# Optimization experiments

Hardware: AMD Instinct MI355X
Metric: run time of the kernel (lower is better)

Reference implementation:

```python
import jax, jax.numpy as jnp
import numpy as np

B, S, D, H, R, N, RK = 2, 2048, 1024, 16, 64, 32, 128
DH = D // H
EPS = 1e-5


def setup_inputs() -> dict:
    key = jax.random.key(0)
    ks = jax.random.split(key, 24)
    f = lambda i, shape, sc=1.0: jax.random.normal(ks[i], shape, dtype=jnp.float32) * sc
    sm = lambda i, shape: jax.nn.softmax(f(i, shape), axis=-1)
    return {
        'x': f(0, (B, S, D)),
        'f_qk': f(1, (N, D, R), 0.02), 'f_v': f(2, (N, D, R), 0.02),
        'r_qk': f(3, (N, R, D), 0.02), 'r_v': f(4, (N, R, D), 0.02),
        'f_know': f(5, (N, D, RK), 0.02), 'r_know': f(6, (N, RK, D), 0.02),
        'W_O': f(7, (D, D), 0.02),
        'gamma1': jnp.ones(D, jnp.float32), 'beta1': jnp.zeros(D, jnp.float32),
        'gamma2': jnp.ones(D, jnp.float32), 'beta2': jnp.zeros(D, jnp.float32),
        'w_fq': sm(8, (B, S, N)), 'w_fk': sm(9, (B, S, N)), 'w_fv': sm(10, (B, S, N)),
        'w_rq': sm(11, (B, S, N)), 'w_rk': sm(12, (B, S, N)), 'w_rv': sm(13, (B, S, N)),
        'w_know_f': sm(14, (B, S, N)), 'w_know_r': sm(15, (B, S, N)),
    }


def _ln(x, g, b):
    mu = jnp.mean(x, axis=-1, keepdims=True)
    var = jnp.mean(jnp.square(x - mu), axis=-1, keepdims=True)
    return g * (x - mu) * jax.lax.rsqrt(var + EPS) + b


def _feature(x, neurons, w):
    # x [B,S,D], neurons [N,D,R], w [B,S,N] -> [B,S,R]
    all_h = jnp.einsum('bsd,ndr->bsnr', x, neurons)
    return jnp.einsum('bsnr,bsn->bsr', all_h, w)


def _restore(h, neurons, w):
    # h [B,S,R], neurons [N,R,D], w [B,S,N] -> [B,S,D]
    # fuse: avoid materializing [B,S,N,D]; outer-product [B,S,N,R] is small
    t = w[..., None] * h[:, :, None, :]
    return jnp.einsum('bsnr,nrd->bsd', t, neurons)


def _causal_attn(Q, K, V):
    # Q,K,V: [B,H,S,DH]
    scale = 1.0 / jnp.sqrt(jnp.asarray(DH, Q.dtype))
    scores = jnp.einsum('bhqd,bhkd->bhqk', Q, K) * scale
    mask = jnp.tril(jnp.ones((S, S), bool))
    scores = jnp.where(mask, scores, jnp.asarray(-jnp.inf, scores.dtype))
    probs = jax.nn.softmax(scores, axis=-1)
    return jnp.einsum('bhqk,bhkd->bhqd', probs, V)


def reference(x, f_qk, f_v, r_qk, r_v, f_know, r_know, W_O,
              gamma1, beta1, gamma2, beta2,
              w_fq, w_fk, w_fv, w_rq, w_rk, w_rv, w_know_f, w_know_r):
    # --- attention circuit ---
    nx = _ln(x, gamma1, beta1)
    h_q = _feature(nx, f_qk, w_fq)
    h_k = _feature(nx, f_qk, w_fk)
    h_v = _feature(nx, f_v, w_fv)
    Q = _restore(h_q, r_qk, w_rq)
    K = _restore(h_k, r_qk, w_rk)
    V = _restore(h_v, r_v, w_rv)
    to_heads = lambda t: t.reshape(B, S, H, DH).transpose(0, 2, 1, 3)
    attn = _causal_attn(to_heads(Q), to_heads(K), to_heads(V))
    attn = attn.transpose(0, 2, 1, 3).reshape(B, S, D)
    attn_out = attn @ W_O.T  # nn.Linear(d_model, d_model, bias=False)
    x = x + attn_out
    # --- knowledge circuit ---
    nx2 = _ln(x, gamma2, beta2)
    h = _feature(nx2, f_know, w_know_f)
    know_out = _restore(h, r_know, w_know_r)
    x = x + know_out
    return x
```

## Files before the change

### kernel.cpp

```cpp
#include <hip/hip_runtime.h>
#include <stdint.h>


typedef __bf16 bf16x8 __attribute__((ext_vector_type(8)));
typedef float f32x4 __attribute__((ext_vector_type(4)));

__device__ __forceinline__ unsigned short f2b(float f) {
  union { float f; unsigned u; } v; v.f = f;
  unsigned u = v.u;
  unsigned r = (u + 0x7FFFu + ((u >> 16) & 1u)) >> 16;
  return (unsigned short)r;
}
__device__ __forceinline__ float b2f(unsigned short h) {
  union { unsigned u; float f; } v; v.u = ((unsigned)h) << 16;
  return v.f;
}
__device__ __forceinline__ unsigned pk2(float lo, float hi) {
  return (unsigned)f2b(lo) | ((unsigned)f2b(hi) << 16);
}
__device__ __forceinline__ unsigned pkt(float lo, float hi) {
  union { float f; unsigned u; } a, b; a.f = lo; b.f = hi;
  return __builtin_amdgcn_perm(b.u, a.u, 0x07060302u);
}
__device__ __forceinline__ f32x4 vmax4(f32x4 a, f32x4 b) {
  f32x4 r;
  r[0] = fmaxf(a[0], b[0]); r[1] = fmaxf(a[1], b[1]);
  r[2] = fmaxf(a[2], b[2]); r[3] = fmaxf(a[3], b[3]);
  return r;
}

#define PHASE(M0) { \
  const bf16x8 a00 = *(const bf16x8*)&lsA[cur][(wr * 128 + (M0) * 16 + l16) * 64 + sl0]; \
  const bf16x8 a01 = *(const bf16x8*)&lsA[cur][(wr * 128 + (M0) * 16 + l16) * 64 + sl1]; \
  const bf16x8 a10 = *(const bf16x8*)&lsA[cur][(wr * 128 + (M0 + 1) * 16 + l16) * 64 + sl0]; \
  const bf16x8 a11 = *(const bf16x8*)&lsA[cur][(wr * 128 + (M0 + 1) * 16 + l16) * 64 + sl1]; \
  __builtin_amdgcn_s_setprio(1); \
  _Pragma("unroll") \
  for (int n = 0; n < 4; ++n) { \
    acc[M0][n] = __builtin_amdgcn_mfma_f32_16x16x32_bf16(a00, bfr[n][0], acc[M0][n], 0, 0, 0); \
    acc[M0][n] = __builtin_amdgcn_mfma_f32_16x16x32_bf16(a01, bfr[n][1], acc[M0][n], 0, 0, 0); \
    acc[M0 + 1][n] = __builtin_amdgcn_mfma_f32_16x16x32_bf16(a10, bfr[n][0], acc[M0 + 1][n], 0, 0, 0); \
    acc[M0 + 1][n] = __builtin_amdgcn_mfma_f32_16x16x32_bf16(a11, bfr[n][1], acc[M0 + 1][n], 0, 0, 0); \
  } \
  __builtin_amdgcn_s_setprio(0); }

__global__ __launch_bounds__(512, 2) void gemm_bt256(
    const unsigned short* __restrict__ A, const unsigned short* __restrict__ Bt,
    unsigned short* __restrict__ out, int K) {
  __shared__ unsigned short lsA[2][256 * 64];
  __shared__ unsigned short lsB[2][256 * 64];
  const int N = 4096;
  const int bid = blockIdx.x;
  const int xcd = bid & 7, j = bid >> 3;
  const int row0 = (xcd * 2 + (j >> 4)) * 256;
  const int col0 = (j & 15) * 256;
  const int tid = threadIdx.x;
  const int w = tid >> 6, lane = tid & 63;
  const int quad = lane >> 4, l16 = lane & 15;
  const int wr = w >> 2, wc = w & 3;

  const int scg = ((lane & 7) ^ (lane >> 3)) * 8;
  const unsigned short* apg = A + (size_t)(row0 + w * 8 + (lane >> 3)) * K + scg;
  const unsigned short* bpg = Bt + (size_t)(col0 + w * 8 + (lane >> 3)) * K + scg;

  const int sl0 = (quad ^ (l16 & 7)) * 8;
  const int sl1 = ((4 + quad) ^ (l16 & 7)) * 8;

  const f32x4 fz = {0.f, 0.f, 0.f, 0.f};
  f32x4 acc[8][4];
#pragma unroll
  for (int m = 0; m < 8; ++m)
#pragma unroll
    for (int n = 0; n < 4; ++n) acc[m][n] = fz;

  auto stA = [&](int b, int i, int k0) {
    __builtin_amdgcn_global_load_lds(
        (const __attribute__((address_space(1))) unsigned int*)(apg + (size_t)(i * 64) * K + k0),
        (__attribute__((address_space(3))) unsigned int*)&lsA[b][(i * 64 + w * 8) * 64],
        16, 0, 0);
  };
  auto stB = [&](int b, int i, int k0) {
    __builtin_amdgcn_global_load_lds(
        (const __attribute__((address_space(1))) unsigned int*)(bpg + (size_t)(i * 64) * K + k0),
        (__attribute__((address_space(3))) unsigned int*)&lsB[b][(i * 64 + w * 8) * 64],
        16, 0, 0);
  };

  const int T = K >> 6;
  stA(0, 0, 0); stA(0, 2, 0);
  stB(0, 0, 0); stB(0, 1, 0); stB(0, 2, 0); stB(0, 3, 0);
  stA(0, 1, 0); stA(0, 3, 0);

  for (int t = 0; t < T; ++t) {
    const int cur = t & 1, nxt = cur ^ 1;
    const int k1 = (t + 1) << 6;
    const bool pf = (t + 1 < T);
    asm volatile("s_waitcnt vmcnt(2)" ::: "memory");
    __builtin_amdgcn_s_barrier();
    if (pf) { stA(nxt, 0, k1); stA(nxt, 2, k1); }
    bf16x8 bfr[4][2];
#pragma unroll
    for (int n = 0; n < 4; ++n) {
      bfr[n][0] = *(const bf16x8*)&lsB[cur][(wc * 64 + n * 16 + l16) * 64 + sl0];
      bfr[n][1] = *(const bf16x8*)&lsB[cur][(wc * 64 + n * 16 + l16) * 64 + sl1];
    }
    PHASE(0)
    if (pf) { stB(nxt, 0, k1); stB(nxt, 1, k1); }
    PHASE(2)
    if (pf) { asm volatile("s_waitcnt vmcnt(4)" ::: "memory"); }
    else    { asm volatile("s_waitcnt vmcnt(0)" ::: "memory"); }
    __builtin_amdgcn_s_barrier();
    if (pf) { stB(nxt, 2, k1); stB(nxt, 3, k1); }
    PHASE(4)
    if (pf) { stA(nxt, 1, k1); stA(nxt, 3, k1); }
    PHASE(6)
  }

  const int rb = row0 + wr * 128;
  const int cb = col0 + wc * 64;
#pragma unroll
  for (int m = 0; m < 8; ++m) {
#pragma unroll
    for (int n = 0; n < 4; ++n) {
      const int r = rb + m * 16 + quad * 4;
      const int c = cb + n * 16 + l16;
#pragma unroll
      for (int i = 0; i < 4; ++i)
        out[(size_t)(r + i) * N + c] = f2b(acc[m][n][i]);
    }
  }
}

__global__ __launch_bounds__(256, 3) void gemm_qkv(
    const unsigned short* __restrict__ t_qk, const unsigned short* __restrict__ t_v,
    const unsigned short* __restrict__ r_qkT, const unsigned short* __restrict__ r_vT,
    unsigned short* __restrict__ QK, unsigned short* __restrict__ VT) {
  __shared__ unsigned short lsA[128 * 64];
  __shared__ unsigned short lsB[128 * 64];
  const int K = 2048;
  const int bid = blockIdx.x;
  const unsigned short* A;
  const unsigned short* Bt;
  int row0, col0, isv;
  if (bid < 256) {
    const int xcd = bid & 7, j = bid >> 3;
    row0 = (xcd * 4 + (j >> 3)) * 128;
    col0 = (j & 7) * 128;
    A = t_v; Bt = r_vT; isv = 1;
  } else {
    const int u = bid - 256;
    const int xcd = u & 7, j = u >> 3;
    row0 = (xcd * 8 + (j >> 3)) * 128;
    col0 = (j & 7) * 128;
    A = t_qk; Bt = r_qkT; isv = 0;
  }
  const int tid = threadIdx.x;
  const int w = tid >> 6, lane = tid & 63;
  const int quad = lane >> 4, l16 = lane & 15;
  const int wr = w >> 1, wc = w & 1;

  const int srow = w * 32 + (lane >> 3);
  const int scg = ((lane & 7) ^ (lane >> 3)) * 8;
  const unsigned short* ap = A + (size_t)(row0 + srow) * K + scg;
  const unsigned short* bp = Bt + (size_t)(col0 + srow) * K + scg;

  const f32x4 fz = {0.f, 0.f, 0.f, 0.f};
  f32x4 acc[4][4];
#pragma unroll
  for (int i = 0; i < 4; ++i)
#pragma unroll
    for (int jj = 0; jj < 4; ++jj) acc[i][jj] = fz;

  for (int k0 = 0; k0 < K; k0 += 64) {
#pragma unroll
    for (int i = 0; i < 4; ++i) {
      __builtin_amdgcn_global_load_lds(
          (const __attribute__((address_space(1))) unsigned int*)(ap + (size_t)i * 8 * K + k0),
          (__attribute__((address_space(3))) unsigned int*)&lsA[(w * 32 + i * 8) * 64],
          16, 0, 0);
      __builtin_amdgcn_global_load_lds(
          (const __attribute__((address_space(1))) unsigned int*)(bp + (size_t)i * 8 * K + k0),
          (__attribute__((address_space(3))) unsigned int*)&lsB[(w * 32 + i * 8) * 64],
          16, 0, 0);
    }
    __syncthreads();
#pragma unroll
    for (int kk = 0; kk < 2; ++kk) {
      bf16x8 af[4], bfr[4];
      const int sl = (((kk * 4 + quad) ^ (l16 & 7)) * 8);
#pragma unroll
      for (int mt = 0; mt < 4; ++mt)
        af[mt] = *(const bf16x8*)&lsA[(wr * 64 + mt * 16 + l16) * 64 + sl];
#pragma unroll
      for (int nt = 0; nt < 4; ++nt)
        bfr[nt] = *(const bf16x8*)&lsB[(wc * 64 + nt * 16 + l16) * 64 + sl];
#pragma unroll
      for (int mt = 0; mt < 4; ++mt)
#pragma unroll
        for (int nt = 0; nt < 4; ++nt)
          acc[mt][nt] = __builtin_amdgcn_mfma_f32_16x16x32_bf16(af[mt], bfr[nt], acc[mt][nt], 0, 0, 0);
    }
    __syncthreads();
  }

  const int rb = row0 + wr * 64;
  const int cb = col0 + wc * 64;
#pragma unroll
  for (int mt = 0; mt < 4; ++mt) {
#pragma unroll
    for (int nt = 0; nt < 4; ++nt) {
      const int r = rb + mt * 16 + quad * 4;
      const int c = cb + nt * 16 + l16;
#pragma unroll
      for (int i = 0; i < 4; ++i) {
        const float v = acc[mt][nt][i];
        if (isv) VT[(size_t)c * 4096 + (r + i)] = f2b(v);
        else QK[(size_t)(r + i) * 1024 + c] = f2b(v);
      }
    }
  }
}

__global__ __launch_bounds__(256, 3) void gemm_ks3(
    const unsigned short* __restrict__ A, const unsigned short* __restrict__ Bt,
    float* __restrict__ p0, float* __restrict__ p1, float* __restrict__ p2) {
  __shared__ unsigned short lsA[128 * 64];
  __shared__ unsigned short lsB[128 * 64];
  const int N = 1024, K = 4096;
  const int bid = blockIdx.x;
  const int xcd = bid & 7, j = bid >> 3;
  const int row_l = j / 24, rem = j % 24;
  const int ks = rem >> 3, col = rem & 7;
  const int row0 = (xcd * 4 + row_l) * 128;
  const int col0 = col * 128;
  const int kbeg = (ks == 0) ? 0 : (ks == 1) ? 1344 : 2688;
  const int kend = (ks == 0) ? 1344 : (ks == 1) ? 2688 : 4096;
  const int tid = threadIdx.x;
  const int w = tid >> 6, lane = tid & 63;
  const int quad = lane >> 4, l16 = lane & 15;
  const int wr = w >> 1, wc = w & 1;

  const int srow = w * 32 + (lane >> 3);
  const int scg = ((lane & 7) ^ (lane >> 3)) * 8;
  const unsigned short* ap = A + (size_t)(row0 + srow) * K + scg;
  const unsigned short* bp = Bt + (size_t)(col0 + srow) * K + scg;

  const f32x4 fz = {0.f, 0.f, 0.f, 0.f};
  f32x4 acc[4][4];
#pragma unroll
  for (int i = 0; i < 4; ++i)
#pragma unroll
    for (int jj = 0; jj < 4; ++jj) acc[i][jj] = fz;

  for (int k0 = kbeg; k0 < kend; k0 += 64) {
#pragma unroll
    for (int i = 0; i < 4; ++i) {
      __builtin_amdgcn_global_load_lds(
          (const __attribute__((address_space(1))) unsigned int*)(ap + (size_t)i * 8 * K + k0),
          (__attribute__((address_space(3))) unsigned int*)&lsA[(w * 32 + i * 8) * 64],
          16, 0, 0);
      __builtin_amdgcn_global_load_lds(
          (const __attribute__((address_space(1))) unsigned int*)(bp + (size_t)i * 8 * K + k0),
          (__attribute__((address_space(3))) unsigned int*)&lsB[(w * 32 + i * 8) * 64],
          16, 0, 0);
    }
    __syncthreads();
#pragma unroll
    for (int kk = 0; kk < 2; ++kk) {
      bf16x8 af[4], bfr[4];
      const int sl = (((kk * 4 + quad) ^ (l16 & 7)) * 8);
#pragma unroll
      for (int mt = 0; mt < 4; ++mt)
        af[mt] = *(const bf16x8*)&lsA[(wr * 64 + mt * 16 + l16) * 64 + sl];
#pragma unroll
      for (int nt = 0; nt < 4; ++nt)
        bfr[nt] = *(const bf16x8*)&lsB[(wc * 64 + nt * 16 + l16) * 64 + sl];
#pragma unroll
      for (int mt = 0; mt < 4; ++mt)
#pragma unroll
        for (int nt = 0; nt < 4; ++nt)
          acc[mt][nt] = __builtin_amdgcn_mfma_f32_16x16x32_bf16(af[mt], bfr[nt], acc[mt][nt], 0, 0, 0);
    }
    __syncthreads();
  }

  float* out = (ks == 0) ? p0 : (ks == 1) ? p1 : p2;
  const int rb = row0 + wr * 64;
  const int cb = col0 + wc * 64;
#pragma unroll
  for (int mt = 0; mt < 4; ++mt) {
#pragma unroll
    for (int nt = 0; nt < 4; ++nt) {
      const int r = rb + mt * 16 + quad * 4;
      const int c = cb + nt * 16 + l16;
#pragma unroll
      for (int i = 0; i < 4; ++i)
        out[(size_t)(r + i) * N + c] = acc[mt][nt][i];
    }
  }
}

__global__ __launch_bounds__(256) void gemm_wo_res(
    const unsigned short* __restrict__ A, const unsigned short* __restrict__ Bt,
    const float* __restrict__ res, float* __restrict__ out) {
  __shared__ unsigned short lsA[128 * 64];
  __shared__ unsigned short lsB[64 * 64];
  const int K = 1024, N = 1024;
  const int bid = blockIdx.x;
  const int xcd = bid & 7, j = bid >> 3;
  const int row0 = (xcd * 4 + (j & 3)) * 128;
  const int col0 = (j >> 2) * 64;
  const int tid = threadIdx.x;
  const int w = tid >> 6, lane = tid & 63;
  const int quad = lane >> 4, l16 = lane & 15;
  const int wr = w >> 1, wc = w & 1;

  const int srowA = w * 32 + (lane >> 3);
  const int srowB = w * 16 + (lane >> 3);
  const int scg = ((lane & 7) ^ (lane >> 3)) * 8;
  const unsigned short* ap = A + (size_t)(row0 + srowA) * K + scg;
  const unsigned short* bp = Bt + (size_t)(col0 + srowB) * K + scg;

  const f32x4 fz = {0.f, 0.f, 0.f, 0.f};
  f32x4 acc[4][2];
#pragma unroll
  for (int i = 0; i < 4; ++i)
#pragma unroll
    for (int jj = 0; jj < 2; ++jj) acc[i][jj] = fz;

  for (int k0 = 0; k0 < K; k0 += 64) {
#pragma unroll
    for (int i = 0; i < 4; ++i)
      __builtin_amdgcn_global_load_lds(
          (const __attribute__((address_space(1))) unsigned int*)(ap + (size_t)i * 8 * K + k0),
          (__attribute__((address_space(3))) unsigned int*)&lsA[(w * 32 + i * 8) * 64],
          16, 0, 0);
#pragma unroll
    for (int i = 0; i < 2; ++i)
      __builtin_amdgcn_global_load_lds(
          (const __attribute__((address_space(1))) unsigned int*)(bp + (size_t)i * 8 * K + k0),
          (__attribute__((address_space(3))) unsigned int*)&lsB[(w * 16 + i * 8) * 64],
          16, 0, 0);
    __syncthreads();
#pragma unroll
    for (int kk = 0; kk < 2; ++kk) {
      bf16x8 af[4], bfr[2];
      const int sl = (((kk * 4 + quad) ^ (l16 & 7)) * 8);
#pragma unroll
      for (int mt = 0; mt < 4; ++mt)
        af[mt] = *(const bf16x8*)&lsA[(wr * 64 + mt * 16 + l16) * 64 + sl];
#pragma unroll
      for (int nt = 0; nt < 2; ++nt)
        bfr[nt] = *(const bf16x8*)&lsB[(wc * 32 + nt * 16 + l16) * 64 + sl];
#pragma unroll
      for (int mt = 0; mt < 4; ++mt)
#pragma unroll
        for (int nt = 0; nt < 2; ++nt)
          acc[mt][nt] = __builtin_amdgcn_mfma_f32_16x16x32_bf16(af[mt], bfr[nt], acc[mt][nt], 0, 0, 0);
    }
    __syncthreads();
  }

  const int rb = row0 + wr * 64;
  const int cb = col0 + wc * 32;
#pragma unroll
  for (int mt = 0; mt < 4; ++mt) {
#pragma unroll
    for (int nt = 0; nt < 2; ++nt) {
      const int r = rb + mt * 16 + quad * 4;
      const int c = cb + nt * 16 + l16;
#pragma unroll
      for (int i = 0; i < 4; ++i)
        out[(size_t)(r + i) * N + c] = acc[mt][nt][i] + res[(size_t)(r + i) * N + c];
    }
  }
}

__global__ __launch_bounds__(256) void reduce_add4(
    const float* __restrict__ p0, const float* __restrict__ p1,
    const float* __restrict__ p2, const float* __restrict__ res,
    float* __restrict__ out) {
  const int i = (blockIdx.x * 256 + threadIdx.x) * 4;
  const f32x4 a = *(const f32x4*)&p0[i];
  const f32x4 b = *(const f32x4*)&p1[i];
  const f32x4 c = *(const f32x4*)&p2[i];
  const f32x4 e = *(const f32x4*)&res[i];
  f32x4 o;
#pragma unroll
  for (int k = 0; k < 4; ++k) o[k] = ((a[k] + b[k]) + c[k]) + e[k];
  *(f32x4*)&out[i] = o;
}

__global__ __launch_bounds__(256) void ln_kernel(
    const float* __restrict__ x, const float* __restrict__ g,
    const float* __restrict__ be, unsigned short* __restrict__ out) {
  __shared__ float sbuf[4];
  const int t = blockIdx.x, tid = threadIdx.x;
  const float* row = x + (size_t)t * 1024;
  float v[4], s = 0.f;
#pragma unroll
  for (int j = 0; j < 4; ++j) { v[j] = row[tid + j * 256]; s += v[j]; }
#pragma unroll
  for (int off = 32; off; off >>= 1) s += __shfl_xor(s, off);
  if ((tid & 63) == 0) sbuf[tid >> 6] = s;
  __syncthreads();
  const float mu = (sbuf[0] + sbuf[1] + sbuf[2] + sbuf[3]) * (1.f / 1024.f);
  __syncthreads();
  float ss = 0.f;
#pragma unroll
  for (int j = 0; j < 4; ++j) { const float d = v[j] - mu; ss += d * d; }
#pragma unroll
  for (int off = 32; off; off >>= 1) ss += __shfl_xor(ss, off);
  if ((tid & 63) == 0) sbuf[tid >> 6] = ss;
  __syncthreads();
  const float var = (sbuf[0] + sbuf[1] + sbuf[2] + sbuf[3]) * (1.f / 1024.f);
  const float rstd = rsqrtf(var + 1e-5f);
  unsigned short* orow = out + (size_t)t * 1024;
#pragma unroll
  for (int j = 0; j < 4; ++j) {
    const int c = tid + j * 256;
    orow[c] = f2b((v[j] - mu) * rstd * g[c] + be[c]);
  }
}

__global__ __launch_bounds__(256) void mix_attn(
    const unsigned short* __restrict__ all_h,
    const float* __restrict__ w_fq, const float* __restrict__ w_fk,
    const float* __restrict__ w_fv, const float* __restrict__ w_rq,
    const float* __restrict__ w_rk, const float* __restrict__ w_rv,
    unsigned short* __restrict__ t_qk, unsigned short* __restrict__ t_v) {
  __shared__ float hq[64], hk[64], hv[64];
  const int t = blockIdx.x, tid = threadIdx.x;
  const int wvi = tid >> 6, lane = tid & 63;
  const unsigned short* row = all_h + (size_t)t * 4096;
  if (wvi < 3) {
    const float* wf = (wvi == 0 ? w_fq : wvi == 1 ? w_fk : w_fv) + (size_t)t * 32;
    const int base = (wvi == 2) ? 2048 : 0;
    float acc = 0.f;
#pragma unroll
    for (int n = 0; n < 32; ++n) acc += wf[n] * b2f(row[base + n * 64 + lane]);
    (wvi == 0 ? hq : wvi == 1 ? hk : hv)[lane] = acc;
  }
  __syncthreads();
  const int n = tid >> 3, r0 = (tid & 7) * 8;
  const float wq = w_rq[(size_t)t * 32 + n];
  const float wk = w_rk[(size_t)t * 32 + n];
  const float wv2 = w_rv[(size_t)t * 32 + n];
  unsigned dq[4], dk[4], dv[4];
#pragma unroll
  for (int jj = 0; jj < 4; ++jj) {
    dq[jj] = pk2(wq * hq[r0 + 2 * jj], wq * hq[r0 + 2 * jj + 1]);
    dk[jj] = pk2(wk * hk[r0 + 2 * jj], wk * hk[r0 + 2 * jj + 1]);
    dv[jj] = pk2(wv2 * hv[r0 + 2 * jj], wv2 * hv[r0 + 2 * jj + 1]);
  }
  *(uint4*)&t_qk[(size_t)t * 2048 + tid * 8] = *(uint4*)dq;
  *(uint4*)&t_qk[(size_t)(4096 + t) * 2048 + tid * 8] = *(uint4*)dk;
  *(uint4*)&t_v[(size_t)t * 2048 + tid * 8] = *(uint4*)dv;
}

__global__ __launch_bounds__(256) void mix_know(
    const unsigned short* __restrict__ all_h, const float* __restrict__ w_f,
    const float* __restrict__ w_r, unsigned short* __restrict__ t_know) {
  __shared__ float h[128];
  const int t = blockIdx.x, tid = threadIdx.x;
  const unsigned short* row = all_h + (size_t)t * 4096;
  if (tid < 128) {
    const float* wf = w_f + (size_t)t * 32;
    float acc = 0.f;
#pragma unroll
    for (int n = 0; n < 32; ++n) acc += wf[n] * b2f(row[n * 128 + tid]);
    h[tid] = acc;
  }
  __syncthreads();
  const int n = tid >> 3, r0 = (tid & 7) * 16;
  const float wn = w_r[(size_t)t * 32 + n];
  unsigned d[8];
#pragma unroll
  for (int jj = 0; jj < 8; ++jj)
    d[jj] = pk2(wn * h[r0 + 2 * jj], wn * h[r0 + 2 * jj + 1]);
  *(uint4*)&t_know[(size_t)t * 4096 + tid * 16] = *(uint4*)d;
  *(uint4*)&t_know[(size_t)t * 4096 + tid * 16 + 8] = *(uint4*)&d[4];
}

__global__ __launch_bounds__(256) void prep_all(
    const float* __restrict__ f_qk, const float* __restrict__ f_v,
    const float* __restrict__ f_know, const float* __restrict__ r_qk,
    const float* __restrict__ r_v, const float* __restrict__ r_know,
    const float* __restrict__ W_O,
    unsigned short* __restrict__ fcomb, unsigned short* __restrict__ fknowT,
    unsigned short* __restrict__ r_qkT, unsigned short* __restrict__ r_vT,
    unsigned short* __restrict__ r_knowT, unsigned short* __restrict__ WO_bf) {
  __shared__ float tile[32][33];
  const int bid = blockIdx.x;
  const int tx = threadIdx.x, ty = threadIdx.y;
  const float* in;
  unsigned short* out;
  int R, C, gx, loc;
  if (bid < 2048)       { in = f_qk;   out = fcomb;                         R = 1024; C = 64;   gx = 2;  loc = bid; }
  else if (bid < 4096)  { in = f_v;    out = fcomb + (size_t)2048 * 1024;   R = 1024; C = 64;   gx = 2;  loc = bid - 2048; }
  else if (bid < 8192)  { in = f_know; out = fknowT;                        R = 1024; C = 128;  gx = 4;  loc = bid - 4096; }
  else if (bid < 10240) { in = r_qk;   out = r_qkT;                         R = 2048; C = 1024; gx = 32; loc = bid - 8192; }
  else if (bid < 12288) { in = r_v;    out = r_vT;                          R = 2048; C = 1024; gx = 32; loc = bid - 10240; }
  else if (bid < 16384) { in = r_know; out = r_knowT;                       R = 4096; C = 1024; gx = 32; loc = bid - 12288; }
  else {
    const int i = ((bid - 16384) * 256 + ty * 32 + tx) * 4;
    const f32x4 v = *(const f32x4*)&W_O[i];
    *(unsigned*)&WO_bf[i] = pk2(v[0], v[1]);
    *(unsigned*)&WO_bf[i + 2] = pk2(v[2], v[3]);
    return;
  }
  const int tiles = gx * (R >> 5);
  const int bb = loc / tiles, rem = loc % tiles;
  const int r0 = (rem / gx) * 32, c0 = (rem % gx) * 32;
  const float* ip = in + (size_t)bb * R * C;
  unsigned short* op = out + (size_t)bb * R * C;
#pragma unroll
  for (int j = 0; j < 4; ++j)
    tile[ty + j * 8][tx] = ip[(size_t)(r0 + ty + j * 8) * C + c0 + tx];
  __syncthreads();
#pragma unroll
  for (int j = 0; j < 4; ++j)
    op[(size_t)(c0 + ty + j * 8) * R + r0 + tx] = f2b(tile[tx][ty + j * 8]);
}

__global__ __launch_bounds__(256) void flash_split(
    const unsigned short* __restrict__ Q, const unsigned short* __restrict__ Kp,
    const unsigned short* __restrict__ VT, unsigned short* __restrict__ O,
    float* __restrict__ Opart, float* __restrict__ ml) {
  __shared__ unsigned short Kls[2][64 * 64];
  __shared__ unsigned short Vls[2][64 * 64];
  const int uidx = 79 - (int)blockIdx.x;
  int uu = uidx, qt = 0, ch = 0;
  for (int q = 0; q < 32; ++q) {
    const int n = (q >> 3) + 1;
    if (uu < n) { qt = q; ch = uu; break; }
    uu -= n;
  }
  const int bh = blockIdx.y;
  const int b = bh >> 4, h = bh & 15;
  const int tid = threadIdx.x;
  const int w = tid >> 6, lane = tid & 63, quad = lane >> 4, l16 = lane & 15;
  const int tb = b * 2048;
  const int qrow = qt * 64 + w * 16;
  const int ktlo = ch * 8;
  const int kthi = min(qt, ch * 8 + 7);
  const float C = 0.18033688f;

  const int srow = (lane >> 3);
  const int scol = ((lane & 7) ^ srow) * 8;

  bf16x8 qf[2];
#pragma unroll
  for (int kk = 0; kk < 2; ++kk)
    qf[kk] = *(const bf16x8*)&Q[(size_t)(tb + qrow + l16) * 1024 + h * 64 + kk * 32 + quad * 8];

  const f32x4 fz = {0.f, 0.f, 0.f, 0.f};
  float m_i = -1e30f, l_i = 0.f;
  f32x4 o_acc[4];
#pragma unroll
  for (int nt = 0; nt < 4; ++nt) o_acc[nt] = fz;

  auto stage = [&](int buf, int kt) {
#pragma unroll
    for (int j = 0; j < 2; ++j) {
      const int rg = (w * 2 + j) * 8 + srow;
      __builtin_amdgcn_global_load_lds(
          (const __attribute__((address_space(1))) unsigned int*)
              (Kp + (size_t)(tb + kt * 64 + rg) * 1024 + h * 64 + scol),
          (__attribute__((address_space(3))) unsigned int*)&Kls[buf][(w * 2 + j) * 8 * 64],
          16, 0, 0);
      __builtin_amdgcn_global_load_lds(
          (const __attribute__((address_space(1))) unsigned int*)
              (VT + (size_t)(h * 64 + rg) * 4096 + tb + kt * 64 + scol),
          (__attribute__((address_space(3))) unsigned int*)&Vls[buf][(w * 2 + j) * 8 * 64],
          16, 0, 0);
    }
  };

  const int srcA = (((quad & 1) * 32 + l16) << 2);
  const int srcB = srcA + 64;
  const bool hiq = (quad >= 2);

  auto pv_block = [&](f32x4* s, bf16x8* vf, const f32x4& rsv) {
    unsigned pk[4][2];
#pragma unroll
    for (int nt = 0; nt < 4; ++nt) {
      pk[nt][0] = pkt(s[nt][0], s[nt][1]);
      pk[nt][1] = pkt(s[nt][2], s[nt][3]);
    }
#pragma unroll
    for (int kk = 0; kk < 2; ++kk) {
      const int ea = 2 * kk, eb = 2 * kk + 1;
      const unsigned u0 = __builtin_amdgcn_ds_bpermute(srcA, pk[ea][0]);
      const unsigned u1 = __builtin_amdgcn_ds_bpermute(srcA, pk[ea][1]);
      const unsigned u2 = __builtin_amdgcn_ds_bpermute(srcB, pk[ea][0]);
      const unsigned u3 = __builtin_amdgcn_ds_bpermute(srcB, pk[ea][1]);
      const unsigned w0 = __builtin_amdgcn_ds_bpermute(srcA, pk[eb][0]);
      const unsigned w1 = __builtin_amdgcn_ds_bpermute(srcA, pk[eb][1]);
      const unsigned w2 = __builtin_amdgcn_ds_bpermute(srcB, pk[eb][0]);
      const unsigned w3 = __builtin_amdgcn_ds_bpermute(srcB, pk[eb][1]);
      unsigned dw[4];
      dw[0] = hiq ? w0 : u0;
      dw[1] = hiq ? w1 : u1;
      dw[2] = hiq ? w2 : u2;
      dw[3] = hiq ? w3 : u3;
      const bf16x8 pf = *(const bf16x8*)dw;
      __builtin_amdgcn_s_setprio(1);
#pragma unroll
      for (int nt = 0; nt < 4; ++nt)
        o_acc[nt] = __builtin_amdgcn_mfma_f32_16x16x32_bf16(vf[kk * 4 + nt], pf, o_acc[nt], 0, 0, 0);
      __builtin_amdgcn_s_setprio(0);
    }
    float rs = (rsv[0] + rsv[1]) + (rsv[2] + rsv[3]);
    rs += __shfl_xor(rs, 16);
    rs += __shfl_xor(rs, 32);
    l_i += rs;
  };

  stage(0, ktlo);
  __syncthreads();
  int buf = 0;

  const bool hasdiag = (ch == (qt >> 3));
  const int ktnd = hasdiag ? kthi - 1 : kthi;

  for (int kt = ktlo; kt <= ktnd; ++kt) {
    if (kt < kthi) stage(buf ^ 1, kt + 1);
    bf16x8 kf[8], vf[8];
#pragma unroll
    for (int kk = 0; kk < 2; ++kk)
#pragma unroll
      for (int nt = 0; nt < 4; ++nt) {
        const int sl = (((kk * 4 + quad) ^ (l16 & 7)) * 8);
        kf[kk * 4 + nt] = *(const bf16x8*)&Kls[buf][(nt * 16 + l16) * 64 + sl];
        vf[kk * 4 + nt] = *(const bf16x8*)&Vls[buf][(nt * 16 + l16) * 64 + sl];
      }

    f32x4 s[4];
    __builtin_amdgcn_s_setprio(1);
#pragma unroll
    for (int nt = 0; nt < 4; ++nt)
      s[nt] = __builtin_amdgcn_mfma_f32_16x16x32_bf16(kf[nt], qf[0], fz, 0, 0, 0);
#pragma unroll
    for (int nt = 0; nt < 4; ++nt)
      s[nt] = __builtin_amdgcn_mfma_f32_16x16x32_bf16(kf[4 + nt], qf[1], s[nt], 0, 0, 0);
    __builtin_amdgcn_s_setprio(0);

    const f32x4 m4 = vmax4(vmax4(s[0], s[1]), vmax4(s[2], s[3]));
    float mx = fmaxf(fmaxf(m4[0], m4[1]), fmaxf(m4[2], m4[3]));
    mx = fmaxf(mx, __shfl_xor(mx, 16));
    mx = fmaxf(mx, __shfl_xor(mx, 32));
    if (!__all(mx <= m_i)) {
      const float mn = fmaxf(m_i, mx);
      const float al = exp2f((m_i - mn) * C);
      m_i = mn;
      l_i *= al;
#pragma unroll
      for (int nt = 0; nt < 4; ++nt) o_acc[nt] *= al;
    }
    const float mC = m_i * C;
    f32x4 rsv = fz;
#pragma unroll
    for (int nt = 0; nt < 4; ++nt) {
      f32x4 e = s[nt] * C - mC;
      f32x4 p;
#pragma unroll
      for (int i = 0; i < 4; ++i) p[i] = exp2f(e[i]);
      s[nt] = p;
      rsv += p;
    }
    pv_block(s, vf, rsv);
    __syncthreads();
    buf ^= 1;
  }

  if (hasdiag) {
    bf16x8 kf[8], vf[8];
#pragma unroll
    for (int kk = 0; kk < 2; ++kk)
#pragma unroll
      for (int nt = 0; nt < 4; ++nt) {
        const int sl = (((kk * 4 + quad) ^ (l16 & 7)) * 8);
        kf[kk * 4 + nt] = *(const bf16x8*)&Kls[buf][(nt * 16 + l16) * 64 + sl];
        vf[kk * 4 + nt] = *(const bf16x8*)&Vls[buf][(nt * 16 + l16) * 64 + sl];
      }
    const int ntmax = w + 1;
    f32x4 s[4];
#pragma unroll
    for (int nt = 0; nt < 4; ++nt) s[nt] = fz;
    __builtin_amdgcn_s_setprio(1);
#pragma unroll
    for (int kk = 0; kk < 2; ++kk)
#pragma unroll
      for (int nt = 0; nt < 4; ++nt)
        if (nt < ntmax)
          s[nt] = __builtin_amdgcn_mfma_f32_16x16x32_bf16(kf[kk * 4 + nt], qf[kk], s[nt], 0, 0, 0);
    __builtin_amdgcn_s_setprio(0);

    const int qloc = w * 16 + l16;
    float mxs[4] = {-1e30f, -1e30f, -1e30f, -1e30f};
#pragma unroll
    for (int nt = 0; nt < 4; ++nt) {
      if (nt >= ntmax) continue;
#pragma unroll
      for (int i = 0; i < 4; ++i) {
        float v = s[nt][i];
        if ((nt * 16 + quad * 4 + i) > qloc) v = -1e30f;
        s[nt][i] = v;
        mxs[nt] = fmaxf(mxs[nt], v);
      }
    }
    float mx = fmaxf(fmaxf(mxs[0], mxs[1]), fmaxf(mxs[2], mxs[3]));
    mx = fmaxf(mx, __shfl_xor(mx, 16));
    mx = fmaxf(mx, __shfl_xor(mx, 32));
    if (!__all(mx <= m_i)) {
      const float mn = fmaxf(m_i, mx);
      const float al = exp2f((m_i - mn) * C);
      m_i = mn;
      l_i *= al;
#pragma unroll
      for (int nt = 0; nt < 4; ++nt) o_acc[nt] *= al;
    }
    const float mC = m_i * C;
    f32x4 rsv = fz;
#pragma unroll
    for (int nt = 0; nt < 4; ++nt) {
      if (nt >= ntmax) { s[nt] = fz; continue; }
      f32x4 e = s[nt] * C - mC;
      f32x4 p;
#pragma unroll
      for (int i = 0; i < 4; ++i) p[i] = exp2f(e[i]);
      s[nt] = p;
      rsv += p;
    }
    pv_block(s, vf, rsv);
  }

  const int nch = (qt >> 3) + 1;
  if (nch == 1) {
    const float inv = 1.0f / l_i;
    unsigned short* orow = O + (size_t)(tb + qrow + l16) * 1024 + h * 64;
#pragma unroll
    for (int nt = 0; nt < 4; ++nt) {
      const unsigned d0 = pk2(o_acc[nt][0] * inv, o_acc[nt][1] * inv);
      const unsigned d1 = pk2(o_acc[nt][2] * inv, o_acc[nt][3] * inv);
      *(unsigned*)&orow[nt * 16 + quad * 4] = d0;
      *(unsigned*)&orow[nt * 16 + quad * 4 + 2] = d1;
    }
  } else {
    const int slot = bh * 80 + uidx;
    const int lq = w * 16 + l16;
    float* op = Opart + ((size_t)slot * 64 + lq) * 64;
#pragma unroll
    for (int nt = 0; nt < 4; ++nt)
      *(f32x4*)&op[nt * 16 + quad * 4] = o_acc[nt];
    if (quad == 0) {
      ml[(size_t)slot * 128 + lq * 2] = m_i;
      ml[(size_t)slot * 128 + lq * 2 + 1] = l_i;
    }
  }
}

__global__ __launch_bounds__(256) void flash_reduce(
    const float* __restrict__ Opart, const float* __restrict__ ml,
    unsigned short* __restrict__ O) {
  const int qt = 8 + blockIdx.x;
  const int bh = blockIdx.y;
  const int b = bh >> 4, h = bh & 15;
  const int j = qt >> 3;
  const int base = 8 * (j * (j + 1) / 2) + (qt - 8 * j) * (j + 1);
  const int nch = j + 1;
  const int tid = threadIdx.x;
  const int lq = tid >> 2, dq = (tid & 3) * 16;
  const float C = 0.18033688f;

  float mc[4], lc[4];
  float m = -1e30f;
#pragma unroll
  for (int c = 0; c < 4; ++c) {
    if (c < nch) {
      const size_t sl = (size_t)(bh * 80 + base + c) * 128 + lq * 2;
      mc[c] = ml[sl];
      lc[c] = ml[sl + 1];
    } else { mc[c] = -1e30f; lc[c] = 0.f; }
    m = fmaxf(m, mc[c]);
  }
  float fac[4], lt = 0.f;
#pragma unroll
  for (int c = 0; c < 4; ++c) {
    fac[c] = (c < nch) ? exp2f((mc[c] - m) * C) : 0.f;
    lt += fac[c] * lc[c];
  }
  const float inv = 1.0f / lt;
  float acc[16];
#pragma unroll
  for (int i = 0; i < 16; ++i) acc[i] = 0.f;
#pragma unroll
  for (int c = 0; c < 4; ++c) {
    if (c >= nch) continue;
    const float* op = Opart + ((size_t)(bh * 80 + base + c) * 64 + lq) * 64 + dq;
#pragma unroll
    for (int i = 0; i < 16; i += 4) {
      const f32x4 v = *(const f32x4*)&op[i];
#pragma unroll
      for (int k = 0; k < 4; ++k) acc[i + k] += fac[c] * v[k];
    }
  }
  unsigned short* orow = O + (size_t)(b * 2048 + qt * 64 + lq) * 1024 + h * 64 + dq;
#pragma unroll
  for (int i = 0; i < 16; i += 2)
    *(unsigned*)&orow[i] = pk2(acc[i] * inv, acc[i + 1] * inv);
}

extern "C" void kernel_launch(void* const* d_in, const int* in_sizes, int n_in,
                              void* d_out, int out_size, void* d_ws, size_t ws_size,
                              hipStream_t stream) {
  (void)in_sizes; (void)n_in; (void)out_size; (void)ws_size;
  const float* x      = (const float*)d_in[0];
  const float* f_qk   = (const float*)d_in[1];
  const float* f_v    = (const float*)d_in[2];
  const float* r_qk   = (const float*)d_in[3];
  const float* r_v    = (const float*)d_in[4];
  const float* f_know = (const float*)d_in[5];
  const float* r_know = (const float*)d_in[6];
  const float* W_O    = (const float*)d_in[7];
  const float* gamma1 = (const float*)d_in[8];
  const float* beta1  = (const float*)d_in[9];
  const float* gamma2 = (const float*)d_in[10];
  const float* beta2  = (const float*)d_in[11];
  const float* w_fq   = (const float*)d_in[12];
  const float* w_fk   = (const float*)d_in[13];
  const float* w_fv   = (const float*)d_in[14];
  const float* w_rq   = (const float*)d_in[15];
  const float* w_rk   = (const float*)d_in[16];
  const float* w_rv   = (const float*)d_in[17];
  const float* w_kf   = (const float*)d_in[18];
  const float* w_kr   = (const float*)d_in[19];

  char* base = (char*)d_ws;
  size_t off = 0;
  auto alloc = [&](size_t b) { char* p = base + off; off += (b + 255) & ~(size_t)255; return p; };
  unsigned short* fcomb   = (unsigned short*)alloc(8388608);
  unsigned short* fknowT  = (unsigned short*)alloc(8388608);
  unsigned short* r_qkT   = (unsigned short*)alloc(4194304);
  unsigned short* r_vT    = (unsigned short*)alloc(4194304);
  unsigned short* r_knowT = (unsigned short*)alloc(8388608);
  unsigned short* WO_bf   = (unsigned short*)alloc(2097152);
  unsigned short* nx_bf   = (unsigned short*)alloc(8388608);
  unsigned short* all_h   = (unsigned short*)alloc(33554432);
  unsigned short* t_qk    = (unsigned short*)alloc(33554432);
  unsigned short* t_v     = (unsigned short*)alloc(16777216);
  unsigned short* QKbuf   = (unsigned short*)alloc(16777216);
  unsigned short* VT      = (unsigned short*)alloc(8388608);
  unsigned short* attn    = (unsigned short*)alloc(8388608);
  float* x1 = (float*)t_v;
  float* Opart = (float*)all_h;
  float* mlbuf = (float*)((char*)all_h + 41943040);
  float* pW0 = (float*)all_h;
  float* pW1 = (float*)((char*)all_h + 16777216);
  float* pW2 = (float*)QKbuf;

  const dim3 blk256(256), blk512(512), blkT(32, 8);

  prep_all<<<17408, blkT, 0, stream>>>(f_qk, f_v, f_know, r_qk, r_v, r_know, W_O,
                                       fcomb, fknowT, r_qkT, r_vT, r_knowT, WO_bf);

  ln_kernel<<<4096, blk256, 0, stream>>>(x, gamma1, beta1, nx_bf);
  gemm_bt256<<<256, blk512, 0, stream>>>(nx_bf, fcomb, all_h, 1024);
  mix_attn<<<4096, blk256, 0, stream>>>(all_h, w_fq, w_fk, w_fv, w_rq, w_rk, w_rv, t_qk, t_v);
  gemm_qkv<<<768, blk256, 0, stream>>>(t_qk, t_v, r_qkT, r_vT, QKbuf, VT);
  flash_split<<<dim3(80, 32), blk256, 0, stream>>>(QKbuf, QKbuf + (size_t)4096 * 1024, VT, attn,
                                                   Opart, mlbuf);
  flash_reduce<<<dim3(24, 32), blk256, 0, stream>>>(Opart, mlbuf, attn);
  gemm_wo_res<<<512, blk256, 0, stream>>>(attn, WO_bf, x, x1);

  ln_kernel<<<4096, blk256, 0, stream>>>(x1, gamma2, beta2, nx_bf);
  gemm_bt256<<<256, blk512, 0, stream>>>(nx_bf, fknowT, all_h, 1024);
  mix_know<<<4096, blk256, 0, stream>>>(all_h, w_kf, w_kr, t_qk);
  gemm_ks3<<<768, blk256, 0, stream>>>(t_qk, r_knowT, pW0, pW1, pW2);
  reduce_add4<<<4096, blk256, 0, stream>>>(pW0, pW1, pW2, x1, (float*)d_out);
}
```

Baseline: 468.2 us.

## Restructure bt256 GEMM into 8-phase pipeline with finer-grained staged loads

Reworks the main bf16 GEMM loop to process two K-tiles per iteration in eight phases. Each phase issues one half-tile global-to-LDS load, then waits on a barrier and lgkmcnt before its MFMA burst. The aim is to spread memory traffic evenly between MFMA clusters and keep more loads in flight (vmcnt 6). It adds many more barriers per iteration, and the loop assumes K is a multiple of 128.

```diff
diff --git a/kernel.cpp b/kernel.cpp
--- a/kernel.cpp
+++ b/kernel.cpp
@@ -29,20 +29,34 @@
   return r;
 }
 
-#define PHASE(M0) { \
-  const bf16x8 a00 = *(const bf16x8*)&lsA[cur][(wr * 128 + (M0) * 16 + l16) * 64 + sl0]; \
-  const bf16x8 a01 = *(const bf16x8*)&lsA[cur][(wr * 128 + (M0) * 16 + l16) * 64 + sl1]; \
-  const bf16x8 a10 = *(const bf16x8*)&lsA[cur][(wr * 128 + (M0 + 1) * 16 + l16) * 64 + sl0]; \
-  const bf16x8 a11 = *(const bf16x8*)&lsA[cur][(wr * 128 + (M0 + 1) * 16 + l16) * 64 + sl1]; \
+#define MFMA_BF16 __builtin_amdgcn_mfma_f32_16x16x32_bf16
+
+#define PHASE8(TB, MQ, STAGE) { \
+  const int ra = (wr * 128 + (MQ) * 32 + l16) * 64; \
+  const bf16x8 a00 = *(const bf16x8*)&lsA[TB][ra + sl0]; \
+  const bf16x8 a01 = *(const bf16x8*)&lsA[TB][ra + sl1]; \
+  const bf16x8 a10 = *(const bf16x8*)&lsA[TB][ra + 16 * 64 + sl0]; \
+  const bf16x8 a11 = *(const bf16x8*)&lsA[TB][ra + 16 * 64 + sl1]; \
+  STAGE; \
+  __builtin_amdgcn_s_barrier(); \
+  asm volatile("s_waitcnt lgkmcnt(0)" ::: "memory"); \
   __builtin_amdgcn_s_setprio(1); \
   _Pragma("unroll") \
   for (int n = 0; n < 4; ++n) { \
-    acc[M0][n] = __builtin_amdgcn_mfma_f32_16x16x32_bf16(a00, bfr[n][0], acc[M0][n], 0, 0, 0); \
-    acc[M0][n] = __builtin_amdgcn_mfma_f32_16x16x32_bf16(a01, bfr[n][1], acc[M0][n], 0, 0, 0); \
-    acc[M0 + 1][n] = __builtin_amdgcn_mfma_f32_16x16x32_bf16(a10, bfr[n][0], acc[M0 + 1][n], 0, 0, 0); \
-    acc[M0 + 1][n] = __builtin_amdgcn_mfma_f32_16x16x32_bf16(a11, bfr[n][1], acc[M0 + 1][n], 0, 0, 0); \
+    acc[(MQ) * 2][n]     = MFMA_BF16(a00, bfr[n][0], acc[(MQ) * 2][n], 0, 0, 0); \
+    acc[(MQ) * 2][n]     = MFMA_BF16(a01, bfr[n][1], acc[(MQ) * 2][n], 0, 0, 0); \
+    acc[(MQ) * 2 + 1][n] = MFMA_BF16(a10, bfr[n][0], acc[(MQ) * 2 + 1][n], 0, 0, 0); \
+    acc[(MQ) * 2 + 1][n] = MFMA_BF16(a11, bfr[n][1], acc[(MQ) * 2 + 1][n], 0, 0, 0); \
   } \
   __builtin_amdgcn_s_setprio(0); }
+
+#define LOADB(TB) { \
+  _Pragma("unroll") \
+  for (int n = 0; n < 4; ++n) { \
+    const int rb_ = (wc * 64 + n * 16 + l16) * 64; \
+    bfr[n][0] = *(const bf16x8*)&lsB[TB][rb_ + sl0]; \
+    bfr[n][1] = *(const bf16x8*)&lsB[TB][rb_ + sl1]; \
+  } }
 
 __global__ __launch_bounds__(512, 2) void gemm_bt256(
     const unsigned short* __restrict__ A, const unsigned short* __restrict__ Bt,
@@ -73,47 +87,55 @@
 #pragma unroll
     for (int n = 0; n < 4; ++n) acc[m][n] = fz;
 
-  auto stA = [&](int b, int i, int k0) {
-    __builtin_amdgcn_global_load_lds(
-        (const __attribute__((address_space(1))) unsigned int*)(apg + (size_t)(i * 64) * K + k0),
-        (__attribute__((address_space(3))) unsigned int*)&lsA[b][(i * 64 + w * 8) * 64],
-        16, 0, 0);
+  auto stA = [&](int b, int h, int k0) {
+#pragma unroll
+    for (int jj = 0; jj < 2; ++jj)
+      __builtin_amdgcn_global_load_lds(
+          (const __attribute__((address_space(1))) unsigned int*)(apg + (size_t)(jj * 128 + h * 64) * K + k0),
+          (__attribute__((address_space(3))) unsigned int*)&lsA[b][(jj * 128 + h * 64 + w * 8) * 64],
+          16, 0, 0);
   };
-  auto stB = [&](int b, int i, int k0) {
-    __builtin_amdgcn_global_load_lds(
-        (const __attribute__((address_space(1))) unsigned int*)(bpg + (size_t)(i * 64) * K + k0),
-        (__attribute__((address_space(3))) unsigned int*)&lsB[b][(i * 64 + w * 8) * 64],
-        16, 0, 0);
+  auto stB = [&](int b, int h, int k0) {
+#pragma unroll
+    for (int jj = 0; jj < 2; ++jj)
+      __builtin_amdgcn_global_load_lds(
+          (const __attribute__((address_space(1))) unsigned int*)(bpg + (size_t)(h * 128 + jj * 64) * K + k0),
+          (__attribute__((address_space(3))) unsigned int*)&lsB[b][(h * 128 + jj * 64 + w * 8) * 64],
+          16, 0, 0);
   };
 
-  const int T = K >> 6;
-  stA(0, 0, 0); stA(0, 2, 0);
-  stB(0, 0, 0); stB(0, 1, 0); stB(0, 2, 0); stB(0, 3, 0);
-  stA(0, 1, 0); stA(0, 3, 0);
-
-  for (int t = 0; t < T; ++t) {
-    const int cur = t & 1, nxt = cur ^ 1;
-    const int k1 = (t + 1) << 6;
-    const bool pf = (t + 1 < T);
-    asm volatile("s_waitcnt vmcnt(2)" ::: "memory");
+  const int P = K >> 7;
+  stB(0, 0, 0); stB(0, 1, 0); stA(0, 0, 0); stA(0, 1, 0);
+  stB(1, 0, 64); stB(1, 1, 64); stA(1, 0, 64);
+
+  bf16x8 bfr[4][2];
+  for (int i = 0; i < P; ++i) {
+    const int kb = (2 * i + 1) << 6;
+    const int ka2 = (2 * i + 2) << 6;
+    const int kb2 = (2 * i + 3) << 6;
+    const bool pf = (i + 1 < P);
+    asm volatile("s_waitcnt vmcnt(6)" ::: "memory");
     __builtin_amdgcn_s_barrier();
-    if (pf) { stA(nxt, 0, k1); stA(nxt, 2, k1); }
-    bf16x8 bfr[4][2];
-#pragma unroll
-    for (int n = 0; n < 4; ++n) {
-      bfr[n][0] = *(const bf16x8*)&lsB[cur][(wc * 64 + n * 16 + l16) * 64 + sl0];
-      bfr[n][1] = *(const bf16x8*)&lsB[cur][(wc * 64 + n * 16 + l16) * 64 + sl1];
-    }
-    PHASE(0)
-    if (pf) { stB(nxt, 0, k1); stB(nxt, 1, k1); }
-    PHASE(2)
-    if (pf) { asm volatile("s_waitcnt vmcnt(4)" ::: "memory"); }
+    LOADB(0)
+    PHASE8(0, 0, stA(1, 1, kb))
+    __builtin_amdgcn_s_barrier();
+    PHASE8(0, 1, if (pf) stB(0, 0, ka2))
+    __builtin_amdgcn_s_barrier();
+    PHASE8(0, 2, if (pf) stB(0, 1, ka2))
+    __builtin_amdgcn_s_barrier();
+    PHASE8(0, 3, if (pf) stA(0, 0, ka2))
+    if (pf) { asm volatile("s_waitcnt vmcnt(6)" ::: "memory"); }
     else    { asm volatile("s_waitcnt vmcnt(0)" ::: "memory"); }
     __builtin_amdgcn_s_barrier();
-    if (pf) { stB(nxt, 2, k1); stB(nxt, 3, k1); }
-    PHASE(4)
-    if (pf) { stA(nxt, 1, k1); stA(nxt, 3, k1); }
-    PHASE(6)
+    LOADB(1)
+    PHASE8(1, 0, if (pf) stA(0, 1, ka2))
+    __builtin_amdgcn_s_barrier();
+    PHASE8(1, 1, if (pf) stB(1, 0, kb2))
+    __builtin_amdgcn_s_barrier();
+    PHASE8(1, 2, if (pf) stB(1, 1, kb2))
+    __builtin_amdgcn_s_barrier();
+    PHASE8(1, 3, if (pf) stA(1, 0, kb2))
+    __builtin_amdgcn_s_barrier();
   }
 
   const int rb = row0 + wr * 128;
```

After: 485.0 us. 3.6% more time.

## Process two key tiles per attention iteration with shared softmax rescale

Applied to the files above, without the earlier changes.

Restructures the causal attention inner loop so each iteration computes scores for two 64-key tiles held in both LDS buffers. It then runs one max and rescale step and one row-sum reduction per pair, and prefetches the next two tiles after a barrier. This halves the barriers, the online-softmax max and shuffle work, and the rescale branches per key tile. In exchange it uses more registers (two score sets and two V fragment sets live at once), which could lower occupancy, and global loads now overlap less with the score computation.

```diff
diff --git a/kernel.cpp b/kernel.cpp
--- a/kernel.cpp
+++ b/kernel.cpp
@@ -581,7 +581,7 @@
   const int srcB = srcA + 64;
   const bool hiq = (quad >= 2);
 
-  auto pv_block = [&](f32x4* s, bf16x8* vf, const f32x4& rsv) {
+  auto pv_half = [&](f32x4* s, bf16x8* vf) {
     unsigned pk[4][2];
 #pragma unroll
     for (int nt = 0; nt < 4; ++nt) {
@@ -611,31 +611,105 @@
         o_acc[nt] = __builtin_amdgcn_mfma_f32_16x16x32_bf16(vf[kk * 4 + nt], pf, o_acc[nt], 0, 0, 0);
       __builtin_amdgcn_s_setprio(0);
     }
+  };
+
+  stage(0, ktlo);
+  if (ktlo + 1 <= kthi) stage(1, ktlo + 1);
+  __syncthreads();
+
+  const bool hasdiag = (ch == (qt >> 3));
+  const int ktnd = hasdiag ? kthi - 1 : kthi;
+
+  int kt = ktlo;
+  for (; kt + 1 <= ktnd; kt += 2) {
+    f32x4 s0[4], s1[4];
+    bf16x8 vf0[8], vf1[8];
+    {
+      bf16x8 kf[8];
+#pragma unroll
+      for (int kk = 0; kk < 2; ++kk)
+#pragma unroll
+        for (int nt = 0; nt < 4; ++nt) {
+          const int sl = (((kk * 4 + quad) ^ (l16 & 7)) * 8);
+          kf[kk * 4 + nt] = *(const bf16x8*)&Kls[0][(nt * 16 + l16) * 64 + sl];
+          vf0[kk * 4 + nt] = *(const bf16x8*)&Vls[0][(nt * 16 + l16) * 64 + sl];
+        }
+      __builtin_amdgcn_s_setprio(1);
+#pragma unroll
+      for (int nt = 0; nt < 4; ++nt)
+        s0[nt] = __builtin_amdgcn_mfma_f32_16x16x32_bf16(kf[nt], qf[0], fz, 0, 0, 0);
+#pragma unroll
+      for (int nt = 0; nt < 4; ++nt)
+        s0[nt] = __builtin_amdgcn_mfma_f32_16x16x32_bf16(kf[4 + nt], qf[1], s0[nt], 0, 0, 0);
+      __builtin_amdgcn_s_setprio(0);
+    }
+    {
+      bf16x8 kf[8];
+#pragma unroll
+      for (int kk = 0; kk < 2; ++kk)
+#pragma unroll
+        for (int nt = 0; nt < 4; ++nt) {
+          const int sl = (((kk * 4 + quad) ^ (l16 & 7)) * 8);
+          kf[kk * 4 + nt] = *(const bf16x8*)&Kls[1][(nt * 16 + l16) * 64 + sl];
+          vf1[kk * 4 + nt] = *(const bf16x8*)&Vls[1][(nt * 16 + l16) * 64 + sl];
+        }
+      __builtin_amdgcn_s_setprio(1);
+#pragma unroll
+      for (int nt = 0; nt < 4; ++nt)
+        s1[nt] = __builtin_amdgcn_mfma_f32_16x16x32_bf16(kf[nt], qf[0], fz, 0, 0, 0);
+#pragma unroll
+      for (int nt = 0; nt < 4; ++nt)
+        s1[nt] = __builtin_amdgcn_mfma_f32_16x16x32_bf16(kf[4 + nt], qf[1], s1[nt], 0, 0, 0);
+      __builtin_amdgcn_s_setprio(0);
+    }
+    __syncthreads();
+    if (kt + 2 <= kthi) stage(0, kt + 2);
+    if (kt + 3 <= kthi) stage(1, kt + 3);
+
+    f32x4 m4 = vmax4(vmax4(s0[0], s0[1]), vmax4(s0[2], s0[3]));
+    m4 = vmax4(m4, vmax4(vmax4(s1[0], s1[1]), vmax4(s1[2], s1[3])));
+    float mx = fmaxf(fmaxf(m4[0], m4[1]), fmaxf(m4[2], m4[3]));
+    mx = fmaxf(mx, __shfl_xor(mx, 16));
+    mx = fmaxf(mx, __shfl_xor(mx, 32));
+    if (!__all(mx <= m_i)) {
+      const float mn = fmaxf(m_i, mx);
+      const float al = exp2f((m_i - mn) * C);
+      m_i = mn;
+      l_i *= al;
+#pragma unroll
+      for (int nt = 0; nt < 4; ++nt) o_acc[nt] *= al;
+    }
+    const float mC = m_i * C;
+    f32x4 rsv = fz;
+#pragma unroll
+    for (int nt = 0; nt < 4; ++nt) {
+      f32x4 e0 = s0[nt] * C - mC;
+      f32x4 e1 = s1[nt] * C - mC;
+      f32x4 p0, p1;
+#pragma unroll
+      for (int i = 0; i < 4; ++i) { p0[i] = exp2f(e0[i]); p1[i] = exp2f(e1[i]); }
+      s0[nt] = p0; s1[nt] = p1;
+      rsv += p0; rsv += p1;
+    }
+    pv_half(s0, vf0);
+    pv_half(s1, vf1);
     float rs = (rsv[0] + rsv[1]) + (rsv[2] + rsv[3]);
     rs += __shfl_xor(rs, 16);
     rs += __shfl_xor(rs, 32);
     l_i += rs;
-  };
-
-  stage(0, ktlo);
-  __syncthreads();
-  int buf = 0;
-
-  const bool hasdiag = (ch == (qt >> 3));
-  const int ktnd = hasdiag ? kthi - 1 : kthi;
-
-  for (int kt = ktlo; kt <= ktnd; ++kt) {
-    if (kt < kthi) stage(buf ^ 1, kt + 1);
+    __syncthreads();
+  }
+
+  if (kt <= ktnd) {
     bf16x8 kf[8], vf[8];
 #pragma unroll
     for (int kk = 0; kk < 2; ++kk)
 #pragma unroll
       for (int nt = 0; nt < 4; ++nt) {
         const int sl = (((kk * 4 + quad) ^ (l16 & 7)) * 8);
-        kf[kk * 4 + nt] = *(const bf16x8*)&Kls[buf][(nt * 16 + l16) * 64 + sl];
-        vf[kk * 4 + nt] = *(const bf16x8*)&Vls[buf][(nt * 16 + l16) * 64 + sl];
+        kf[kk * 4 + nt] = *(const bf16x8*)&Kls[0][(nt * 16 + l16) * 64 + sl];
+        vf[kk * 4 + nt] = *(const bf16x8*)&Vls[0][(nt * 16 + l16) * 64 + sl];
       }
-
     f32x4 s[4];
     __builtin_amdgcn_s_setprio(1);
 #pragma unroll
@@ -669,20 +743,23 @@
       s[nt] = p;
       rsv += p;
     }
-    pv_block(s, vf, rsv);
-    __syncthreads();
-    buf ^= 1;
+    pv_half(s, vf);
+    float rs = (rsv[0] + rsv[1]) + (rsv[2] + rsv[3]);
+    rs += __shfl_xor(rs, 16);
+    rs += __shfl_xor(rs, 32);
+    l_i += rs;
   }
 
   if (hasdiag) {
+    const int dbuf = (kthi - ktlo) & 1;
     bf16x8 kf[8], vf[8];
 #pragma unroll
     for (int kk = 0; kk < 2; ++kk)
 #pragma unroll
       for (int nt = 0; nt < 4; ++nt) {
         const int sl = (((kk * 4 + quad) ^ (l16 & 7)) * 8);
-        kf[kk * 4 + nt] = *(const bf16x8*)&Kls[buf][(nt * 16 + l16) * 64 + sl];
-        vf[kk * 4 + nt] = *(const bf16x8*)&Vls[buf][(nt * 16 + l16) * 64 + sl];
+        kf[kk * 4 + nt] = *(const bf16x8*)&Kls[dbuf][(nt * 16 + l16) * 64 + sl];
+        vf[kk * 4 + nt] = *(const bf16x8*)&Vls[dbuf][(nt * 16 + l16) * 64 + sl];
       }
     const int ntmax = w + 1;
     f32x4 s[4];
@@ -733,7 +810,11 @@
       s[nt] = p;
       rsv += p;
     }
-    pv_block(s, vf, rsv);
+    pv_half(s, vf);
+    float rs = (rsv[0] + rsv[1]) + (rsv[2] + rsv[3]);
+    rs += __shfl_xor(rs, 16);
+    rs += __shfl_xor(rs, 32);
+    l_i += rs;
   }
 
   const int nch = (qt >> 3) + 1;
```

Result: no change. 473.5 us (+1.1%).
